# Kernel tuning notes

Hardware: AMD Instinct MI355X
Metric: run time of the kernel (lower is better)

The kernel has to match this reference:

```python
import jax, jax.numpy as jnp
import numpy as np

DIM = 512
D_STATE = 16
D_CONV = 4
EXPAND = 2
D_INNER = EXPAND * DIM  # 1024
BATCH = 4
SEQLEN = 4096


def silu(v):
    return v * jax.nn.sigmoid(v)


def setup_inputs() -> dict:
    key = jax.random.key(0)
    ks = jax.random.split(key, 8)
    s = 0.02  # small init scale for stability
    return {
        "x": jax.random.normal(ks[0], (BATCH, SEQLEN, DIM), jnp.float32),
        "W_in": jax.random.normal(ks[1], (2 * D_INNER, DIM), jnp.float32) * s,
        "conv_w": jax.random.normal(ks[2], (D_INNER, 1, D_CONV), jnp.float32) * s,
        "conv_b": jax.random.normal(ks[3], (D_INNER,), jnp.float32) * s,
        "W_x": jax.random.normal(ks[4], (2 * D_STATE, D_INNER), jnp.float32) * s,
        "W_dt": jax.random.normal(ks[5], (D_STATE, D_INNER), jnp.float32) * s,
        "b_dt": jax.random.normal(ks[6], (D_STATE,), jnp.float32) * s,
        "A_log": jnp.log(jnp.arange(1, D_STATE + 1, dtype=jnp.float32))[None, :],
        "D_param": jnp.ones((D_INNER,), jnp.float32),
        "W_out": jax.random.normal(ks[7], (DIM, D_INNER), jnp.float32) * s,
    }


def reference(x, W_in, conv_w, conv_b, W_x, W_dt, b_dt, A_log, D_param, W_out):
    B, L, _ = x.shape
    # in_proj and split into x / res streams
    x_and_res = jnp.einsum('bld,ed->ble', x, W_in)          # [B,L,2*d_inner]
    xi, res = x_and_res[..., :D_INNER], x_and_res[..., D_INNER:]
    # causal depthwise conv1d (torch pads both sides by d_conv-1 then slices [:L]
    # == left-pad d_conv-1, no right pad)
    xc = jax.lax.conv_general_dilated(
        xi.transpose(0, 2, 1), conv_w, (1,), [(D_CONV - 1, 0)],
        dimension_numbers=('NCH', 'OIH', 'NCH'), feature_group_count=D_INNER)
    xa = silu(xc.transpose(0, 2, 1) + conv_b)               # [B,L,d_inner]
    # x_proj: first d_state (dt) half is discarded in the source; keep B half
    B_proj = jnp.einsum('bld,ed->ble', xa, W_x)[..., D_STATE:]  # [B,L,N]
    dt = jax.nn.softplus(jnp.einsum('bld,nd->bln', xa, W_dt) + b_dt)  # [B,L,N]
    A = -jnp.exp(A_log.reshape(-1))                         # [N]
    A_disc = jnp.exp(A * dt)                                # [B,L,N]
    d_rep = D_INNER // D_STATE
    u = jnp.mean(xa[..., :d_rep], axis=-1)                  # [B,L] scalar drive
    Bu = (dt * B_proj) * u[..., None]                       # [B,L,N]

    def step(s, ab):
        a, b = ab
        s = s * a + b
        return s, s

    s0 = jnp.zeros((B, D_STATE), xa.dtype)
    _, y = jax.lax.scan(step, s0, (A_disc.transpose(1, 0, 2), Bu.transpose(1, 0, 2)))
    y = y.transpose(1, 0, 2)                                # [B,L,N]
    y = jnp.repeat(y, d_rep, axis=-1)                       # [B,L,d_inner]
    y = y + xa * D_param
    y = y * silu(res)
    return jnp.einsum('bld,ed->ble', y, W_out)              # [B,L,dim]
```

## Files before the change

### kernel.cpp

```cpp
#include <hip/hip_runtime.h>
#include <stdint.h>

typedef __bf16 bf16_t;
typedef __bf16 bf16x8 __attribute__((ext_vector_type(8)));
typedef __bf16 bf16x4 __attribute__((ext_vector_type(4)));
typedef float  f32x4  __attribute__((ext_vector_type(4)));

#define AS1 __attribute__((address_space(1)))
#define AS3 __attribute__((address_space(3)))

#define SEQ   4096
#define DIMM  512
#define DIN   1024
#define ROWS  16384

__device__ __forceinline__ void gload_lds16(const void* g, void* l) {
  __builtin_amdgcn_global_load_lds((AS1 void*)g, (AS3 void*)l, 16, 0, 0);
}

__global__ __launch_bounds__(512, 2) void gemm8(
    const bf16_t* __restrict__ A, const bf16_t* __restrict__ B,
    bf16_t* __restrict__ C, int lda, int ldb, int N, int K)
{
  __shared__ __align__(16) bf16_t Abuf[4][256*32];
  __shared__ __align__(16) bf16_t Bbuf[4][256*32];
  const int tid = threadIdx.x;
  const int l = tid & 63, w = tid >> 6;
  const int wr = w >> 2, wc = w & 3;
  const int lr = l & 15, g = l >> 4;
  const int bm = blockIdx.x, bn = blockIdx.y;
  const int NT = K >> 5;

  const int r0  = tid >> 2;
  const int c0e = ((tid & 3) ^ ((tid >> 3) & 3)) * 8;
  const bf16_t* As0 = A + (size_t)(bm*256 +       r0)*lda + c0e;
  const bf16_t* As1 = A + (size_t)(bm*256 + 128 + r0)*lda + c0e;
  const bf16_t* Bs0 = B + (size_t)(bn*256 +       r0)*ldb + c0e;
  const bf16_t* Bs1 = B + (size_t)(bn*256 + 128 + r0)*ldb + c0e;

  f32x4 acc[8][4] = {};

#define STAGE_A(kt_) { int d_ = (kt_) & 3; size_t ko_ = (size_t)(kt_)*32; \
    gload_lds16(As0 + ko_, &Abuf[d_][w*512]); \
    gload_lds16(As1 + ko_, &Abuf[d_][4096 + w*512]); }
#define STAGE_B(kt_) { int d_ = (kt_) & 3; size_t ko_ = (size_t)(kt_)*32; \
    gload_lds16(Bs0 + ko_, &Bbuf[d_][w*512]); \
    gload_lds16(Bs1 + ko_, &Bbuf[d_][4096 + w*512]); }

  STAGE_A(0); STAGE_B(0);
  STAGE_A(1); STAGE_B(1);
  asm volatile("s_waitcnt vmcnt(4)" ::: "memory");
  __builtin_amdgcn_s_barrier();
  __builtin_amdgcn_sched_barrier(0);

  const int arow = wr*128 + lr;
  const int brow = wc*64  + lr;
  const int kcol = (g ^ ((lr >> 1) & 3)) * 8;

  for (int kt = 0; kt < NT; ++kt) {
    const bf16_t* Ab = Abuf[kt & 3];
    const bf16_t* Bb = Bbuf[kt & 3];
    bf16x8 av[4], bv[4];
#pragma unroll
    for (int m = 0; m < 4; m++) av[m] = *(const bf16x8*)&Ab[(arow + m*16)*32 + kcol];
#pragma unroll
    for (int n = 0; n < 4; n++) bv[n] = *(const bf16x8*)&Bb[(brow + n*16)*32 + kcol];
    if (kt + 2 < NT) STAGE_A(kt + 2);
    asm volatile("s_waitcnt lgkmcnt(0)" ::: "memory");
    __builtin_amdgcn_sched_barrier(0);
    __builtin_amdgcn_s_setprio(1);
#pragma unroll
    for (int m = 0; m < 4; m++)
#pragma unroll
      for (int n = 0; n < 4; n++)
        acc[m][n] = __builtin_amdgcn_mfma_f32_16x16x32_bf16(av[m], bv[n], acc[m][n], 0, 0, 0);
    __builtin_amdgcn_s_setprio(0);
    __builtin_amdgcn_sched_barrier(0);
#pragma unroll
    for (int m = 0; m < 4; m++) av[m] = *(const bf16x8*)&Ab[(arow + 64 + m*16)*32 + kcol];
    if (kt + 2 < NT) STAGE_B(kt + 2);
    asm volatile("s_waitcnt lgkmcnt(0)" ::: "memory");
    __builtin_amdgcn_sched_barrier(0);
    __builtin_amdgcn_s_setprio(1);
#pragma unroll
    for (int m = 0; m < 4; m++)
#pragma unroll
      for (int n = 0; n < 4; n++)
        acc[4+m][n] = __builtin_amdgcn_mfma_f32_16x16x32_bf16(av[m], bv[n], acc[4+m][n], 0, 0, 0);
    __builtin_amdgcn_s_setprio(0);
    __builtin_amdgcn_sched_barrier(0);
    if (kt < NT - 1) {
      if (kt + 2 < NT) asm volatile("s_waitcnt vmcnt(4)" ::: "memory");
      else             asm volatile("s_waitcnt vmcnt(0)" ::: "memory");
      __builtin_amdgcn_s_barrier();
      __builtin_amdgcn_sched_barrier(0);
    }
  }
#undef STAGE_A
#undef STAGE_B

  const int row0 = bm*256 + wr*128 + g*4;
  const int col0 = bn*256 + wc*64 + lr;
#pragma unroll
  for (int m = 0; m < 8; m++)
#pragma unroll
    for (int n = 0; n < 4; n++)
#pragma unroll
      for (int r = 0; r < 4; r++)
        C[(size_t)(row0 + m*16 + r)*N + col0 + n*16] = (bf16_t)acc[m][n][r];
}

template<int MODE>
__global__ void gemm_bt(const bf16_t* __restrict__ A, const bf16_t* __restrict__ B,
                        void* __restrict__ Cv, int lda, int N, int K,
                        const float* __restrict__ u_g, const float* __restrict__ b_dt_g,
                        const float* __restrict__ A_log_g)
{
  __shared__ __align__(16) bf16_t As[128*64];
  __shared__ __align__(16) bf16_t Bs[128*64];
  const int tid = threadIdx.x;
  const int l = tid & 63, w = tid >> 6;
  const int bm = blockIdx.x, bn = blockIdx.y;
  const bf16_t* Ab = A + (size_t)bm*128*lda;
  const bf16_t* Bb = B + (size_t)bn*128*K;
  f32x4 acc[4][4] = {};
  const int wr = (w>>1)*64, wc = (w&1)*64;
  const int lr = l & 15;
  const int srow = w*8 + (l>>3);
  const int scol = ((tid&7) ^ ((tid>>3)&7)) * 8;
  const int lk0  = ((l>>4) ^ (l&7)) * 8;
  const int lk1  = lk0 ^ 32;

  for (int kt = 0; kt < K; kt += 64) {
#pragma unroll
    for (int i = 0; i < 4; i++) {
      gload_lds16(Ab + (size_t)(i*32 + srow)*lda + kt + scol, As + i*2048 + w*512);
      gload_lds16(Bb + (size_t)(i*32 + srow)*K   + kt + scol, Bs + i*2048 + w*512);
    }
    __syncthreads();
#pragma unroll
    for (int kk = 0; kk < 2; kk++) {
      const int lk = kk ? lk1 : lk0;
      bf16x8 af[4], bv[4];
#pragma unroll
      for (int m = 0; m < 4; m++) af[m] = *(const bf16x8*)&As[(wr + m*16 + lr)*64 + lk];
#pragma unroll
      for (int n = 0; n < 4; n++) bv[n] = *(const bf16x8*)&Bs[(wc + n*16 + lr)*64 + lk];
#pragma unroll
      for (int m = 0; m < 4; m++)
#pragma unroll
        for (int n = 0; n < 4; n++)
          acc[m][n] = __builtin_amdgcn_mfma_f32_16x16x32_bf16(af[m], bv[n], acc[m][n], 0, 0, 0);
    }
    __syncthreads();
  }
  const int row0 = bm*128 + wr + (l>>4)*4;
  const int col0 = bn*128 + wc + lr;

  if constexpr (MODE == 2) {
    if (wc == 0) {
      const float bdt  = b_dt_g[lr];
      const float Aexp = expf(A_log_g[lr]);
      float2* aBu = (float2*)Cv;
#pragma unroll
      for (int m = 0; m < 4; m++)
#pragma unroll
        for (int r = 0; r < 4; r++) {
          int row = row0 + m*16 + r;
          float xdt = acc[m][0][r] + bdt;
          float dt  = (xdt > 20.f) ? xdt : log1pf(expf(xdt));
          float a   = expf(-Aexp * dt);
          float Bu  = dt * acc[m][1][r] * u_g[row];
          int b = row >> 12, li = row & 4095;
          aBu[(size_t)((b<<4) + lr)*4096 + li] = make_float2(a, Bu);
        }
    }
    return;
  }

#pragma unroll
  for (int m = 0; m < 4; m++)
#pragma unroll
    for (int n = 0; n < 4; n++)
#pragma unroll
      for (int r = 0; r < 4; r++) {
        size_t idx = (size_t)(row0 + m*16 + r)*N + (col0 + n*16);
        ((float*)Cv)[idx] = acc[m][n][r];
      }
}

__global__ __launch_bounds__(256) void convert_kernel(
    const float* __restrict__ x, const float* __restrict__ W_in,
    const float* __restrict__ W_out, const float* __restrict__ W_dt, const float* __restrict__ W_x,
    bf16_t* __restrict__ x_bf, bf16_t* __restrict__ Win_bf,
    bf16_t* __restrict__ Wout_bf, bf16_t* __restrict__ Wcat_bf)
{
  const size_t N0 = 8388608/4, N1 = N0 + 1048576/4, N2 = N1 + 524288/4, N3 = N2 + 131072/4;
  size_t i = (size_t)blockIdx.x*256 + threadIdx.x;
  bf16_t* dst; float4 v;
  if (i < N0)      { v = ((const float4*)x)[i];          dst = x_bf   + i*4; }
  else if (i < N1) { size_t j = i - N0; v = ((const float4*)W_in)[j];  dst = Win_bf  + j*4; }
  else if (i < N2) { size_t j = i - N1; v = ((const float4*)W_out)[j]; dst = Wout_bf + j*4; }
  else if (i < N3) {
    size_t j = i - N2; size_t el = j*4; int r = (int)(el >> 10), c = (int)(el & 1023);
    if (r < 16)      v = *(const float4*)(W_dt + r*1024 + c);
    else if (r < 32) v = *(const float4*)(W_x  + r*1024 + c);
    else             v = make_float4(0.f, 0.f, 0.f, 0.f);
    dst = Wcat_bf + el;
  } else return;
  bf16x4 o; o[0]=(bf16_t)v.x; o[1]=(bf16_t)v.y; o[2]=(bf16_t)v.z; o[3]=(bf16_t)v.w;
  *(bf16x4*)dst = o;
}

#define CONV_R 4
__global__ __launch_bounds__(256) void conv_kernel(
    const bf16_t* __restrict__ xi_res, const float* __restrict__ conv_w,
    const float* __restrict__ conv_b, bf16_t* __restrict__ xa, float* __restrict__ u)
{
  const int team = blockIdx.x*2 + (threadIdx.x >> 7);
  const int t    = threadIdx.x & 127;
  const int b    = team >> 10;
  const int r0   = (team & 1023) * CONV_R;
  const int c0   = t * 8;

  float w[8][4], bias[8];
#pragma unroll
  for (int e = 0; e < 8; e++) {
    float4 v = *(const float4*)(conv_w + (size_t)(c0 + e)*4);
    w[e][0]=v.x; w[e][1]=v.y; w[e][2]=v.z; w[e][3]=v.w;
  }
  {
    float4 b0 = *(const float4*)(conv_b + c0);
    float4 b1 = *(const float4*)(conv_b + c0 + 4);
    bias[0]=b0.x; bias[1]=b0.y; bias[2]=b0.z; bias[3]=b0.w;
    bias[4]=b1.x; bias[5]=b1.y; bias[6]=b1.z; bias[7]=b1.w;
  }

  const bf16_t* xbase = xi_res + ((size_t)b*SEQ + r0)*2048 + c0;
  bf16x8 rowv[CONV_R + 3];
#pragma unroll
  for (int k = 0; k < 3; k++) {
#pragma unroll
    for (int e = 0; e < 8; e++) rowv[k][e] = (bf16_t)0.f;
    if (r0 - 3 + k >= 0) rowv[k] = *(const bf16x8*)(xbase + (k - 3)*2048);
  }
#pragma unroll
  for (int k = 0; k < CONV_R; k++)
    rowv[3 + k] = *(const bf16x8*)(xbase + k*2048);

  const int growbase = b*SEQ + r0;
#pragma unroll
  for (int i = 0; i < CONV_R; i++) {
    bf16x8 o;
    float usum = 0.f;
#pragma unroll
    for (int e = 0; e < 8; e++) {
      float acc = bias[e]
        + w[e][0]*(float)rowv[i  ][e]
        + w[e][1]*(float)rowv[i+1][e]
        + w[e][2]*(float)rowv[i+2][e]
        + w[e][3]*(float)rowv[i+3][e];
      float sil = acc / (1.f + expf(-acc));
      usum += sil;
      o[e] = (bf16_t)sil;
    }
    *(bf16x8*)(xa + (size_t)(growbase + i)*DIN + c0) = o;
    if (t < 8) {
      usum += __shfl_xor(usum, 1, 64);
      usum += __shfl_xor(usum, 2, 64);
      usum += __shfl_xor(usum, 4, 64);
      if (t == 0) u[growbase + i] = usum * (1.f/64.f);
    }
  }
}

__global__ __launch_bounds__(256) void scan_kernel(const float2* __restrict__ aBu, float* __restrict__ y)
{
  __shared__ float2 lds[4096 + 256];
  __shared__ float2 wtot[4];
  const int tid = threadIdx.x;
  const int bn = blockIdx.x;
  const float2* base = aBu + (size_t)bn*4096;

#pragma unroll
  for (int c = 0; c < 16; c++) {
    int i = c*256 + tid;
    lds[i + (i>>4)] = base[i];
  }
  __syncthreads();

  const int p0 = tid*17;
  float P = 1.f, S = 0.f;
#pragma unroll
  for (int j = 0; j < 16; j++) {
    float2 ab = lds[p0 + j];
    S = S*ab.x + ab.y;
    P *= ab.x;
  }
  float Pi = P, Si = S;
  const int l = tid & 63;
#pragma unroll
  for (int off = 1; off < 64; off <<= 1) {
    float Pp = __shfl_up(Pi, off, 64);
    float Sp = __shfl_up(Si, off, 64);
    if (l >= off) { Si = Sp*Pi + Si; Pi = Pp*Pi; }
  }
  const int w = tid >> 6;
  if (l == 63) wtot[w] = make_float2(Pi, Si);
  __syncthreads();

  float Sc = 0.f;
  for (int k = 0; k < 4; k++)
    if (k < w) { Sc = Sc*wtot[k].x + wtot[k].y; }
  float Pe = 1.f, Se = 0.f;
  {
    float Pp = __shfl_up(Pi, 1, 64);
    float Sp = __shfl_up(Si, 1, 64);
    if (l > 0) { Pe = Pp; Se = Sp; }
  }
  float s = Sc*Pe + Se;

#pragma unroll
  for (int j = 0; j < 16; j++) {
    float2 ab = lds[p0 + j];
    s = s*ab.x + ab.y;
    lds[p0 + j].x = s;
  }
  __syncthreads();
  float* yb = y + (size_t)bn*4096;
#pragma unroll
  for (int c = 0; c < 16; c++) {
    int i = c*256 + tid;
    yb[i] = lds[i + (i>>4)].x;
  }
}

__global__ __launch_bounds__(256) void yfull_kernel(
    const bf16_t* __restrict__ xa, bf16_t* __restrict__ xi_res,
    const float* __restrict__ y_state, const float* __restrict__ D_param)
{
  int idx = blockIdx.x*256 + threadIdx.x;
  int row = idx >> 7, cc = (idx & 127)*8;
  bf16x8 xav  = *(const bf16x8*)&xa[(size_t)row*DIN + cc];
  bf16x8 resv = *(const bf16x8*)&xi_res[(size_t)row*2048 + DIN + cc];
  int b = row >> 12, li = row & 4095, n = cc >> 6;
  float ys = y_state[(size_t)((b<<4) + n)*4096 + li];
  float dp[8];
  float4 d0 = *(const float4*)(D_param + cc);
  float4 d1 = *(const float4*)(D_param + cc + 4);
  dp[0]=d0.x; dp[1]=d0.y; dp[2]=d0.z; dp[3]=d0.w; dp[4]=d1.x; dp[5]=d1.y; dp[6]=d1.z; dp[7]=d1.w;
  bf16x8 o;
#pragma unroll
  for (int e = 0; e < 8; e++) {
    float r = (float)resv[e];
    float sil = r / (1.f + expf(-r));
    float yv = (ys + (float)xav[e]*dp[e]) * sil;
    o[e] = (bf16_t)yv;
  }
  *(bf16x8*)&xi_res[(size_t)row*2048 + cc] = o;
}

extern "C" void kernel_launch(void* const* d_in, const int* in_sizes, int n_in,
                              void* d_out, int out_size, void* d_ws, size_t ws_size,
                              hipStream_t stream)
{
  const float* x      = (const float*)d_in[0];
  const float* W_in   = (const float*)d_in[1];
  const float* conv_w = (const float*)d_in[2];
  const float* conv_b = (const float*)d_in[3];
  const float* W_x    = (const float*)d_in[4];
  const float* W_dt   = (const float*)d_in[5];
  const float* b_dt   = (const float*)d_in[6];
  const float* A_log  = (const float*)d_in[7];
  const float* D_param= (const float*)d_in[8];
  const float* W_out  = (const float*)d_in[9];
  float* out = (float*)d_out;
  char* ws = (char*)d_ws;

  if (ws_size < 121700352u) return;

  const size_t MB = 1024*1024;
  bf16_t* x_bf    = (bf16_t*)(ws + 0);
  float*  y_state = (float*) (ws + 8*MB);
  bf16_t* Win_bf  = (bf16_t*)(ws + 16*MB);
  float2* aBu     = (float2*)(ws + 16*MB);
  bf16_t* Wout_bf = (bf16_t*)(ws + 18*MB);
  bf16_t* Wcat_bf = (bf16_t*)(ws + 19*MB);
  bf16_t* xi_res  = (bf16_t*)(ws + 20*MB);
  bf16_t* xa      = (bf16_t*)(ws + 84*MB);
  float*  u       = (float*) (ws + 116*MB);

  convert_kernel<<<dim3(9856), dim3(256), 0, stream>>>(x, W_in, W_out, W_dt, W_x,
                                                       x_bf, Win_bf, Wout_bf, Wcat_bf);
  gemm8<<<dim3(64, 8), dim3(512), 0, stream>>>(x_bf, Win_bf, xi_res, 512, 512, 2048, 512);
  conv_kernel<<<dim3(2048), dim3(256), 0, stream>>>(xi_res, conv_w, conv_b, xa, u);
  gemm_bt<2><<<dim3(128,1), dim3(256), 0, stream>>>(xa, Wcat_bf, (void*)aBu, 1024, 128, 1024,
                                                    u, b_dt, A_log);
  scan_kernel<<<dim3(64), dim3(256), 0, stream>>>(aBu, y_state);
  yfull_kernel<<<dim3(8192), dim3(256), 0, stream>>>(xa, xi_res, y_state, D_param);
  gemm_bt<0><<<dim3(128,4), dim3(256), 0, stream>>>(xi_res, Wout_bf, (void*)out, 2048, 512, 1024,
                                                    nullptr, nullptr, nullptr);
}
```

Measured before the change: 229.3 us.

## Fuse gated y computation into out-projection GEMM and shrink in-proj pipeline depth

Removes the separate yfull kernel and computes y = (y_state + xa*D) * silu(res) while loading the A tile inside a new out-projection GEMM. This avoids writing and re-reading the gated y tensor through global memory. The in-projection GEMM also drops from a 4-stage to a 2-stage LDS buffer with launch bounds raised to allow more resident blocks, at the cost of less prefetch depth and a full vmcnt(0) wait every iteration. The new GEMM does no software pipelining, so the elementwise work and the loads sit in series with the MFMAs, and the gated values are recomputed once per N tile (four times).

Result: slower. 567.5 us (+147.4%).

```diff
diff --git a/kernel.cpp b/kernel.cpp
--- a/kernel.cpp
+++ b/kernel.cpp
@@ -18,12 +18,14 @@
   __builtin_amdgcn_global_load_lds((AS1 void*)g, (AS3 void*)l, 16, 0, 0);
 }
 
-__global__ __launch_bounds__(512, 2) void gemm8(
+__device__ __forceinline__ float silu_f(float v) { return v / (1.f + expf(-v)); }
+
+__global__ __launch_bounds__(512, 4) void gemm8(
     const bf16_t* __restrict__ A, const bf16_t* __restrict__ B,
     bf16_t* __restrict__ C, int lda, int ldb, int N, int K)
 {
-  __shared__ __align__(16) bf16_t Abuf[4][256*32];
-  __shared__ __align__(16) bf16_t Bbuf[4][256*32];
+  __shared__ __align__(16) bf16_t Abuf[2][256*32];
+  __shared__ __align__(16) bf16_t Bbuf[2][256*32];
   const int tid = threadIdx.x;
   const int l = tid & 63, w = tid >> 6;
   const int wr = w >> 2, wc = w & 3;
@@ -40,16 +42,15 @@
 
   f32x4 acc[8][4] = {};
 
-#define STAGE_A(kt_) { int d_ = (kt_) & 3; size_t ko_ = (size_t)(kt_)*32; \
+#define STAGE_A(kt_) { int d_ = (kt_) & 1; size_t ko_ = (size_t)(kt_)*32; \
     gload_lds16(As0 + ko_, &Abuf[d_][w*512]); \
     gload_lds16(As1 + ko_, &Abuf[d_][4096 + w*512]); }
-#define STAGE_B(kt_) { int d_ = (kt_) & 3; size_t ko_ = (size_t)(kt_)*32; \
+#define STAGE_B(kt_) { int d_ = (kt_) & 1; size_t ko_ = (size_t)(kt_)*32; \
     gload_lds16(Bs0 + ko_, &Bbuf[d_][w*512]); \
     gload_lds16(Bs1 + ko_, &Bbuf[d_][4096 + w*512]); }
 
   STAGE_A(0); STAGE_B(0);
-  STAGE_A(1); STAGE_B(1);
-  asm volatile("s_waitcnt vmcnt(4)" ::: "memory");
+  asm volatile("s_waitcnt vmcnt(0)" ::: "memory");
   __builtin_amdgcn_s_barrier();
   __builtin_amdgcn_sched_barrier(0);
 
@@ -58,14 +59,14 @@
   const int kcol = (g ^ ((lr >> 1) & 3)) * 8;
 
   for (int kt = 0; kt < NT; ++kt) {
-    const bf16_t* Ab = Abuf[kt & 3];
-    const bf16_t* Bb = Bbuf[kt & 3];
+    const bf16_t* Ab = Abuf[kt & 1];
+    const bf16_t* Bb = Bbuf[kt & 1];
     bf16x8 av[4], bv[4];
 #pragma unroll
     for (int m = 0; m < 4; m++) av[m] = *(const bf16x8*)&Ab[(arow + m*16)*32 + kcol];
 #pragma unroll
     for (int n = 0; n < 4; n++) bv[n] = *(const bf16x8*)&Bb[(brow + n*16)*32 + kcol];
-    if (kt + 2 < NT) STAGE_A(kt + 2);
+    if (kt + 1 < NT) STAGE_A(kt + 1);
     asm volatile("s_waitcnt lgkmcnt(0)" ::: "memory");
     __builtin_amdgcn_sched_barrier(0);
     __builtin_amdgcn_s_setprio(1);
@@ -78,7 +79,7 @@
     __builtin_amdgcn_sched_barrier(0);
 #pragma unroll
     for (int m = 0; m < 4; m++) av[m] = *(const bf16x8*)&Ab[(arow + 64 + m*16)*32 + kcol];
-    if (kt + 2 < NT) STAGE_B(kt + 2);
+    if (kt + 1 < NT) STAGE_B(kt + 1);
     asm volatile("s_waitcnt lgkmcnt(0)" ::: "memory");
     __builtin_amdgcn_sched_barrier(0);
     __builtin_amdgcn_s_setprio(1);
@@ -90,8 +91,7 @@
     __builtin_amdgcn_s_setprio(0);
     __builtin_amdgcn_sched_barrier(0);
     if (kt < NT - 1) {
-      if (kt + 2 < NT) asm volatile("s_waitcnt vmcnt(4)" ::: "memory");
-      else             asm volatile("s_waitcnt vmcnt(0)" ::: "memory");
+      asm volatile("s_waitcnt vmcnt(0)" ::: "memory");
       __builtin_amdgcn_s_barrier();
       __builtin_amdgcn_sched_barrier(0);
     }
@@ -187,6 +187,76 @@
         size_t idx = (size_t)(row0 + m*16 + r)*N + (col0 + n*16);
         ((float*)Cv)[idx] = acc[m][n][r];
       }
+}
+
+__global__ __launch_bounds__(256) void gemm_yg(
+    const bf16_t* __restrict__ xa, const bf16_t* __restrict__ xi_res,
+    const float* __restrict__ y_state, const float* __restrict__ D_param,
+    const bf16_t* __restrict__ B, float* __restrict__ C, int N, int K)
+{
+  __shared__ __align__(16) bf16_t As[128*64];
+  __shared__ __align__(16) bf16_t Bs[128*64];
+  const int tid = threadIdx.x;
+  const int l = tid & 63, w = tid >> 6;
+  const int bm = blockIdx.x, bn = blockIdx.y;
+  const bf16_t* Bb = B + (size_t)bn*128*K;
+  f32x4 acc[4][4] = {};
+  const int wr = (w>>1)*64, wc = (w&1)*64;
+  const int lr = l & 15;
+  const int srow = w*8 + (l>>3);
+  const int slog = (tid&7) ^ ((tid>>3)&7);
+  const int scol = slog * 8;
+  const int lk0  = ((l>>4) ^ (l&7)) * 8;
+  const int lk1  = lk0 ^ 32;
+
+  for (int kt = 0; kt < K; kt += 64) {
+    const int kg = kt + scol;
+    const int n16 = kg >> 6;
+    float4 d0 = *(const float4*)(D_param + kg);
+    float4 d1 = *(const float4*)(D_param + kg + 4);
+    float dp[8] = {d0.x,d0.y,d0.z,d0.w,d1.x,d1.y,d1.z,d1.w};
+#pragma unroll
+    for (int i = 0; i < 4; i++) {
+      const int row_g = bm*128 + i*32 + srow;
+      const int b = row_g >> 12, li = row_g & 4095;
+      bf16x8 xav  = *(const bf16x8*)&xa[(size_t)row_g*DIN + kg];
+      bf16x8 resv = *(const bf16x8*)&xi_res[(size_t)row_g*2048 + DIN + kg];
+      float ys = y_state[(size_t)((b<<4) + n16)*4096 + li];
+      bf16x8 o;
+#pragma unroll
+      for (int e = 0; e < 8; e++) {
+        float yv = (ys + (float)xav[e]*dp[e]) * silu_f((float)resv[e]);
+        o[e] = (bf16_t)yv;
+      }
+      *(bf16x8*)&As[i*2048 + w*512 + l*8] = o;
+      gload_lds16(Bb + (size_t)(i*32 + srow)*K + kt + scol, Bs + i*2048 + w*512);
+    }
+    __syncthreads();
+#pragma unroll
+    for (int kk = 0; kk < 2; kk++) {
+      const int lk = kk ? lk1 : lk0;
+      bf16x8 af[4], bv[4];
+#pragma unroll
+      for (int m = 0; m < 4; m++) af[m] = *(const bf16x8*)&As[(wr + m*16 + lr)*64 + lk];
+#pragma unroll
+      for (int n = 0; n < 4; n++) bv[n] = *(const bf16x8*)&Bs[(wc + n*16 + lr)*64 + lk];
+#pragma unroll
+      for (int m = 0; m < 4; m++)
+#pragma unroll
+        for (int n = 0; n < 4; n++)
+          acc[m][n] = __builtin_amdgcn_mfma_f32_16x16x32_bf16(af[m], bv[n], acc[m][n], 0, 0, 0);
+    }
+    __syncthreads();
+  }
+  const int row0 = bm*128 + wr + (l>>4)*4;
+  const int col0 = bn*128 + wc + lr;
+#pragma unroll
+  for (int m = 0; m < 4; m++)
+#pragma unroll
+    for (int n = 0; n < 4; n++)
+#pragma unroll
+      for (int r = 0; r < 4; r++)
+        C[(size_t)(row0 + m*16 + r)*N + col0 + n*16] = acc[m][n][r];
 }
 
 __global__ __launch_bounds__(256) void convert_kernel(
@@ -260,7 +330,7 @@
         + w[e][1]*(float)rowv[i+1][e]
         + w[e][2]*(float)rowv[i+2][e]
         + w[e][3]*(float)rowv[i+3][e];
-      float sil = acc / (1.f + expf(-acc));
+      float sil = silu_f(acc);
       usum += sil;
       o[e] = (bf16_t)sil;
     }
@@ -333,31 +403,6 @@
     int i = c*256 + tid;
     yb[i] = lds[i + (i>>4)].x;
   }
-}
-
-__global__ __launch_bounds__(256) void yfull_kernel(
-    const bf16_t* __restrict__ xa, bf16_t* __restrict__ xi_res,
-    const float* __restrict__ y_state, const float* __restrict__ D_param)
-{
-  int idx = blockIdx.x*256 + threadIdx.x;
-  int row = idx >> 7, cc = (idx & 127)*8;
-  bf16x8 xav  = *(const bf16x8*)&xa[(size_t)row*DIN + cc];
-  bf16x8 resv = *(const bf16x8*)&xi_res[(size_t)row*2048 + DIN + cc];
-  int b = row >> 12, li = row & 4095, n = cc >> 6;
-  float ys = y_state[(size_t)((b<<4) + n)*4096 + li];
-  float dp[8];
-  float4 d0 = *(const float4*)(D_param + cc);
-  float4 d1 = *(const float4*)(D_param + cc + 4);
-  dp[0]=d0.x; dp[1]=d0.y; dp[2]=d0.z; dp[3]=d0.w; dp[4]=d1.x; dp[5]=d1.y; dp[6]=d1.z; dp[7]=d1.w;
-  bf16x8 o;
-#pragma unroll
-  for (int e = 0; e < 8; e++) {
-    float r = (float)resv[e];
-    float sil = r / (1.f + expf(-r));
-    float yv = (ys + (float)xav[e]*dp[e]) * sil;
-    o[e] = (bf16_t)yv;
-  }
-  *(bf16x8*)&xi_res[(size_t)row*2048 + cc] = o;
 }
 
 extern "C" void kernel_launch(void* const* d_in, const int* in_sizes, int n_in,
@@ -397,7 +442,6 @@
   gemm_bt<2><<<dim3(128,1), dim3(256), 0, stream>>>(xa, Wcat_bf, (void*)aBu, 1024, 128, 1024,
                                                     u, b_dt, A_log);
   scan_kernel<<<dim3(64), dim3(256), 0, stream>>>(aBu, y_state);
-  yfull_kernel<<<dim3(8192), dim3(256), 0, stream>>>(xa, xi_res, y_state, D_param);
-  gemm_bt<0><<<dim3(128,4), dim3(256), 0, stream>>>(xi_res, Wout_bf, (void*)out, 2048, 512, 1024,
-                                                    nullptr, nullptr, nullptr);
-}
+  gemm_yg<<<dim3(128,4), dim3(256), 0, stream>>>(xa, xi_res, y_state, D_param,
+                                                 Wout_bf, out, 512, 1024);
+}
```
